# Performance work log

Hardware: AMD Instinct MI355X
Metric: run time of the kernel (lower is better)

The kernel has to match this reference:

```python
import jax, jax.numpy as jnp
import numpy as np

N_CLASS, EMB, HID = 10000, 512, 1024
BATCH, SEQ = 64, 128

_W_NAMES = [
    ("C", (N_CLASS, EMB)),
    ("W_fx", (EMB, HID)), ("W_fh", (HID, HID)),
    ("W_ix", (EMB, HID)), ("W_ih", (HID, HID)),
    ("W_Cx", (EMB, HID)), ("W_Ch", (HID, HID)),
    ("W_ox", (EMB, HID)), ("W_oh", (HID, HID)),
    ("W_fx1", (HID, HID)), ("W_fh1", (HID, HID)),
    ("W_ix1", (HID, HID)), ("W_ih1", (HID, HID)),
    ("W_Cx1", (HID, HID)), ("W_Ch1", (HID, HID)),
    ("W_ox1", (HID, HID)), ("W_oh1", (HID, HID)),
    ("W_out", (HID, N_CLASS)),
]
_B_NAMES = [("b_f", HID), ("b_i", HID), ("b_C", HID), ("b_o", HID),
            ("b_f1", HID), ("b_i1", HID), ("b_C1", HID), ("b_o1", HID),
            ("b_out", N_CLASS)]


def setup_inputs() -> dict:
    key = jax.random.key(0)
    inp = {"X": jax.random.randint(jax.random.fold_in(key, 0), (BATCH, SEQ), 0, N_CLASS)}
    for i, (name, shape) in enumerate(_W_NAMES):
        inp[name] = 0.02 * jax.random.normal(jax.random.fold_in(key, 100 + i), shape, jnp.float32)
    for name, n in _B_NAMES:
        inp[name] = jnp.ones((n,), jnp.float32)  # original inits biases to ones
    return inp


def reference(X, C, W_fx, W_fh, W_ix, W_ih, W_Cx, W_Ch, W_ox, W_oh,
              W_fx1, W_fh1, W_ix1, W_ih1, W_Cx1, W_Ch1, W_ox1, W_oh1,
              W_out, b_f, b_i, b_C, b_o, b_f1, b_i1, b_C1, b_o1, b_out):
    E = jnp.swapaxes(C[X], 0, 1)              # [S, B, emb]
    B = X.shape[0]
    h0 = jnp.zeros((B, W_fh.shape[0]), E.dtype)

    # Layer 0: precompute all input-side gate projections (batched GEMMs).
    xg0 = (E @ W_fx, E @ W_ix, E @ W_Cx, E @ W_ox)  # each [S, B, H]

    def step0(carry, xs):
        h, c = carry
        xf, xi, xc, xo = xs
        f = jax.nn.sigmoid(xf + h @ W_fh + b_f)
        i = jax.nn.sigmoid(xi + h @ W_ih + b_i)
        g = jnp.tanh(xc + h @ W_Ch + b_C)
        c = f * c + i * g
        o = jax.nn.sigmoid(xo + h @ W_oh + b_o)
        h = o * jnp.tanh(c)
        return (h, c), h

    _, H = jax.lax.scan(step0, (h0, h0), xg0)  # H: [S, B, H]

    # Layer 1 (NOTE: original code reuses layer-0 W_ih in the i-gate — kept).
    xg1 = (H @ W_fx1, H @ W_ix1, H @ W_Cx1, H @ W_ox1)

    def step1(carry, xs):
        h, c = carry
        xf, xi, xc, xo = xs
        f = jax.nn.sigmoid(xf + h @ W_fh1 + b_f1)
        i = jax.nn.sigmoid(xi + h @ W_ih + b_i1)
        g = jnp.tanh(xc + h @ W_Ch1 + b_C1)
        c = f * c + i * g
        o = jax.nn.sigmoid(xo + h @ W_oh1 + b_o1)
        h = o * jnp.tanh(c)
        return (h, c), None

    (h1, _), _ = jax.lax.scan(step1, (h0, h0), xg1)
    return h1 @ W_out + b_out                 # [B, n_class]
```

## Files before the change

kernel.cpp:

```cpp
#include <hip/hip_runtime.h>
#include <cstdint>
#include <cstddef>

#define BATCH 64
#define SEQ   128
#define EMB   512
#define HID   1024
#define NCLS  10000
#define NG    4096
#define NOP   10048
#define BH    (BATCH * HID)

typedef __attribute__((ext_vector_type(8))) short short8;
typedef __attribute__((ext_vector_type(4))) short short4v;
typedef __attribute__((ext_vector_type(4))) float floatx4;
typedef unsigned short u16;
typedef unsigned char  u8;

#define RED_PAD    36
#define LDS_BYTES  (8 * 64 * RED_PAD * 4)

__device__ __forceinline__ u16 f2bf(float x) {
    union { float f; unsigned u; } v; v.f = x;
    unsigned r = v.u + 0x7fffu + ((v.u >> 16) & 1u);
    return (u16)(r >> 16);
}
__device__ __forceinline__ float sigm(float x) { return 1.f / (1.f + __expf(-x)); }

__device__ __forceinline__ void wave_wait_range(const unsigned* lines, int lo,
                                                int n, unsigned tgt) {
    const int ln = threadIdx.x & 63;
    const unsigned* p = lines + (size_t)(lo + ln) * 16;
    for (;;) {
        bool ok = true;
        if (ln < n) {
            unsigned v = __hip_atomic_load(p, __ATOMIC_RELAXED, __HIP_MEMORY_SCOPE_AGENT);
            ok = ((v & 255u) >= tgt) && (((v >> 8) & 255u) >= tgt) &&
                 (((v >> 16) & 255u) >= tgt) && ((v >> 24) >= tgt);
        }
        if (__all(ok)) break;
        __builtin_amdgcn_s_sleep(1);
    }
}

__global__ void pack_gates(const float* __restrict__ s0, const float* __restrict__ s1,
                           const float* __restrict__ s2, const float* __restrict__ s3,
                           u16* __restrict__ dst, int kgroups, int kg_off) {
    int t = blockIdx.x * blockDim.x + threadIdx.x;
    if (t >= kgroups * HID) return;
    int u  = t & (HID - 1);
    int kg = t >> 10;
    u16* out = dst + ((size_t)(kg + kg_off) * NG + (size_t)u * 4) * 8;
#pragma unroll
    for (int g = 0; g < 4; ++g) {
        const float* s = (g == 0) ? s0 : (g == 1) ? s1 : (g == 2) ? s2 : s3;
        short8 v;
#pragma unroll
        for (int j = 0; j < 8; ++j)
            v[j] = (short)f2bf(s[(size_t)(kg * 8 + j) * HID + u]);
        *(short8*)(out + g * 8) = v;
    }
}

__global__ void pack_wout(const float* __restrict__ src, u16* __restrict__ dst) {
    int t = blockIdx.x * blockDim.x + threadIdx.x;
    if (t >= 128 * NCLS) return;
    int n  = t % NCLS;
    int kg = t / NCLS;
    short8 v;
#pragma unroll
    for (int j = 0; j < 8; ++j)
        v[j] = (short)f2bf(src[(size_t)(kg * 8 + j) * NCLS + n]);
    *(short8*)(dst + ((size_t)kg * NOP + n) * 8) = v;
}

__global__ void embed_k(const int* __restrict__ X, const float* __restrict__ C,
                        u16* __restrict__ E) {
    const int sb = blockIdx.x;
    const int s = sb >> 6, m = sb & 63;
    const int row = X[m * SEQ + s];
    const floatx4* src = (const floatx4*)(C + (size_t)row * EMB);
    const int t = threadIdx.x;
    floatx4 v = src[t];
    short4v o;
    o[0] = (short)f2bf(v[0]); o[1] = (short)f2bf(v[1]);
    o[2] = (short)f2bf(v[2]); o[3] = (short)f2bf(v[3]);
    u16* dst = E + (size_t)s * (64 * 512) + (size_t)(t >> 1) * 512 + m * 8 + (t & 1) * 4;
    *(short4v*)dst = o;
}

template<int NS, bool WRITE_H>
__device__ __forceinline__ void compute_tick(
    float* __restrict__ redf,
    const short8 (&wreg)[NS][2],
    const short8 (&areg)[NS][4],
    u16* __restrict__ ho, u16* __restrict__ Hout,
    float& c, float bF, float bI, float bC, float bO, int ub)
{
    const int tid = threadIdx.x;
    const int kw = tid >> 6, l = tid & 63;
    const int ml = l & 15, q = l >> 4;

    floatx4 acc[4][2];
#pragma unroll
    for (int mt = 0; mt < 4; ++mt)
#pragma unroll
        for (int ch = 0; ch < 2; ++ch)
            acc[mt][ch] = (floatx4){0.f, 0.f, 0.f, 0.f};

#pragma unroll
    for (int ci = 0; ci < NS; ++ci)
#pragma unroll
        for (int mt = 0; mt < 4; ++mt) {
            acc[mt][0] = __builtin_amdgcn_mfma_f32_16x16x32_bf16(
                areg[ci][mt], wreg[ci][0], acc[mt][0], 0, 0, 0);
            acc[mt][1] = __builtin_amdgcn_mfma_f32_16x16x32_bf16(
                areg[ci][mt], wreg[ci][1], acc[mt][1], 0, 0, 0);
        }

#pragma unroll
    for (int mt = 0; mt < 4; ++mt)
#pragma unroll
        for (int ch = 0; ch < 2; ++ch)
#pragma unroll
            for (int r = 0; r < 4; ++r)
                redf[((size_t)kw * 64 + mt * 16 + q * 4 + r) * RED_PAD + ch * 16 + ml]
                    = acc[mt][ch][r];
    __syncthreads();

    const int m = tid >> 3, u = tid & 7;
    const int nl = u * 4;
    float p0 = 0.f, p1 = 0.f, p2 = 0.f, p3 = 0.f;
#pragma unroll
    for (int k2 = 0; k2 < 8; ++k2) {
        floatx4 rv = *(const floatx4*)&redf[((size_t)k2 * 64 + m) * RED_PAD + nl];
        p0 += rv[0]; p1 += rv[1]; p2 += rv[2]; p3 += rv[3];
    }
    float f = sigm(p0 + bF);
    float i = sigm(p1 + bI);
    float g = tanhf(p2 + bC);
    float o = sigm(p3 + bO);
    float cc = f * c + i * g;
    c = cc;
    u16 hb = f2bf(o * tanhf(cc));
    __hip_atomic_store(&ho[(size_t)ub * 512 + tid], hb,
                       __ATOMIC_RELAXED, __HIP_MEMORY_SCOPE_AGENT);
    if (WRITE_H)
        __hip_atomic_store(&Hout[(size_t)ub * 512 + tid], hb,
                           __ATOMIC_RELAXED, __HIP_MEMORY_SCOPE_AGENT);
}

struct PArgs {
    const u16 *E, *Wcat0, *Wcat1;
    u16 *H, *h0c, *h1c;
    const float *b_f, *b_i, *b_C, *b_o, *b_f1, *b_i1, *b_C1, *b_o1;
    unsigned* sync;
};

__global__ void __launch_bounds__(512, 2) persist_k(PArgs a) {
    extern __shared__ float redf[];

    const int b   = blockIdx.x;
    const int ub  = b & 127;
    const int tid = threadIdx.x;
    const bool L0 = (b < 128);

    const int kw = tid >> 6, l = tid & 63;
    const int ml = l & 15, q = l >> 4;

    const int ug = ub * 8 + (tid & 7);
    const float bF = L0 ? a.b_f[ug] : a.b_f1[ug];
    const float bI = L0 ? a.b_i[ug] : a.b_i1[ug];
    const float bC = L0 ? a.b_C[ug] : a.b_C1[ug];
    const float bO = L0 ? a.b_o[ug] : a.b_o1[ug];
    float c = 0.f;

    unsigned* flags0_u32 = a.sync;
    unsigned* flags1_u32 = a.sync + 1024;
    u8* my0 = (u8*)a.sync + (size_t)(ub >> 2) * 64 + (ub & 3);
    u8* my1 = (u8*)a.sync + 4096 + (size_t)(ub >> 2) * 64 + (ub & 3);

    if (L0) {
        short8 wreg[6][2];
#pragma unroll
        for (int ci = 0; ci < 6; ++ci)
#pragma unroll
            for (int ch = 0; ch < 2; ++ch) {
                const int kg = (kw * 6 + ci) * 4 + q;
                wreg[ci][ch] = *(const short8*)(
                    a.Wcat0 + ((size_t)kg * NG + ub * 32 + ch * 16 + ml) * 8);
            }
        const int Sl   = kw * 6 + 5;
        const bool hasH = (Sl >= 16);
        const int flo  = (kw * 6 > 16) ? (kw * 6 - 16) : 0;
        const int fcnt = hasH ? (Sl - 16 - flo + 1) : 0;

        for (int t = 0; t < 128; ++t) {
            short8 areg[6][4];
            const u16* Et  = a.E   + (size_t)t * (64 * 512);
            const u16* hin = a.h0c + (size_t)t * BH;
#pragma unroll
            for (int ci = 0; ci < 6; ++ci) {
                const int S = kw * 6 + ci;
                if (S < 16) {
                    const int kg = S * 4 + q;
#pragma unroll
                    for (int mt = 0; mt < 4; ++mt)
                        areg[ci][mt] = *(const short8*)(
                            Et + (size_t)kg * 512 + (mt * 16 + ml) * 8);
                }
            }
            if (hasH && t > 0) wave_wait_range(flags0_u32, flo, fcnt, (unsigned)t);
            asm volatile("" ::: "memory");
#pragma unroll
            for (int ci = 0; ci < 6; ++ci) {
                const int S = kw * 6 + ci;
                if (S >= 16) {
                    const int kg = (S - 16) * 4 + q;
#pragma unroll
                    for (int mt = 0; mt < 4; ++mt)
                        areg[ci][mt] = *(const short8*)(
                            hin + (size_t)kg * 512 + (mt * 16 + ml) * 8);
                }
            }
            __builtin_amdgcn_sched_barrier(0);
            compute_tick<6, true>(redf, wreg, areg,
                                  a.h0c + (size_t)(t + 1) * BH,
                                  a.H + (size_t)t * BH,
                                  c, bF, bI, bC, bO, ub);
            asm volatile("s_waitcnt vmcnt(0)" ::: "memory");
            __syncthreads();
            if (tid == 0)
                __hip_atomic_store(my0, (u8)(t + 1),
                                   __ATOMIC_RELAXED, __HIP_MEMORY_SCOPE_AGENT);
        }
    } else {
        short8 wreg[8][2];
#pragma unroll
        for (int ci = 0; ci < 8; ++ci)
#pragma unroll
            for (int ch = 0; ch < 2; ++ch) {
                const int kg = (kw * 8 + ci) * 4 + q;
                wreg[ci][ch] = *(const short8*)(
                    a.Wcat1 + ((size_t)kg * NG + ub * 32 + ch * 16 + ml) * 8);
            }
        const int kg0 = (kw & 3) * 8;

        for (int s = 0; s < 128; ++s) {
            short8 areg[8][4];
            const u16* src;
            if (kw >= 4) {
                if (s > 0) wave_wait_range(flags1_u32, kg0, 8, (unsigned)s);
                src = a.h1c + (size_t)s * BH;
            } else {
                wave_wait_range(flags0_u32, kg0, 8, (unsigned)(s + 1));
                src = a.H + (size_t)s * BH;
            }
            asm volatile("" ::: "memory");
#pragma unroll
            for (int ci = 0; ci < 8; ++ci) {
                const int kg = (kg0 + ci) * 4 + q;
#pragma unroll
                for (int mt = 0; mt < 4; ++mt)
                    areg[ci][mt] = *(const short8*)(
                        src + (size_t)kg * 512 + (mt * 16 + ml) * 8);
            }
            __builtin_amdgcn_sched_barrier(0);
            compute_tick<8, false>(redf, wreg, areg,
                                   a.h1c + (size_t)(s + 1) * BH, nullptr,
                                   c, bF, bI, bC, bO, ub);
            asm volatile("s_waitcnt vmcnt(0)" ::: "memory");
            __syncthreads();
            if (tid == 0)
                __hip_atomic_store(my1, (u8)(s + 1),
                                   __ATOMIC_RELAXED, __HIP_MEMORY_SCOPE_AGENT);
        }
    }
}

__global__ void __launch_bounds__(256) out_gemm(
    const u16* __restrict__ h1, const u16* __restrict__ W,
    const float* __restrict__ bout, float* __restrict__ out)
{
    __shared__ float red[4][64][33];
    const int tid = threadIdx.x;
    const int w = tid >> 6, l = tid & 63;
    const int ml = l & 15, q = l >> 4;
    const int n0 = blockIdx.x * 32;

    floatx4 acc[4][2];
#pragma unroll
    for (int mi = 0; mi < 4; ++mi)
#pragma unroll
        for (int ni = 0; ni < 2; ++ni)
            acc[mi][ni] = (floatx4){0.f, 0.f, 0.f, 0.f};

#pragma unroll
    for (int ci = 0; ci < 8; ++ci) {
        const int k = (ci * 4 + w) << 5;
        const int kg = (k >> 3) + q;
        const u16* ar = h1 + (size_t)kg * 512 + ml * 8;
        short8 a0 = *(const short8*)(ar);
        short8 a1 = *(const short8*)(ar + 16 * 8);
        short8 a2 = *(const short8*)(ar + 32 * 8);
        short8 a3 = *(const short8*)(ar + 48 * 8);
        const u16* br = W + ((size_t)((k >> 3) + q) * NOP + n0 + ml) * 8;
        short8 b0 = *(const short8*)(br);
        short8 b1 = *(const short8*)(br + 16 * 8);
        acc[0][0] = __builtin_amdgcn_mfma_f32_16x16x32_bf16(a0, b0, acc[0][0], 0, 0, 0);
        acc[1][0] = __builtin_amdgcn_mfma_f32_16x16x32_bf16(a1, b0, acc[1][0], 0, 0, 0);
        acc[2][0] = __builtin_amdgcn_mfma_f32_16x16x32_bf16(a2, b0, acc[2][0], 0, 0, 0);
        acc[3][0] = __builtin_amdgcn_mfma_f32_16x16x32_bf16(a3, b0, acc[3][0], 0, 0, 0);
        acc[0][1] = __builtin_amdgcn_mfma_f32_16x16x32_bf16(a0, b1, acc[0][1], 0, 0, 0);
        acc[1][1] = __builtin_amdgcn_mfma_f32_16x16x32_bf16(a1, b1, acc[1][1], 0, 0, 0);
        acc[2][1] = __builtin_amdgcn_mfma_f32_16x16x32_bf16(a2, b1, acc[2][1], 0, 0, 0);
        acc[3][1] = __builtin_amdgcn_mfma_f32_16x16x32_bf16(a3, b1, acc[3][1], 0, 0, 0);
    }

#pragma unroll
    for (int mi = 0; mi < 4; ++mi)
#pragma unroll
        for (int ni = 0; ni < 2; ++ni)
#pragma unroll
            for (int r = 0; r < 4; ++r)
                red[w][mi * 16 + q * 4 + r][ni * 16 + ml] = acc[mi][ni][r];
    __syncthreads();

    const int m = tid >> 2;
#pragma unroll
    for (int jj = 0; jj < 8; ++jj) {
        const int nl = (tid & 3) * 8 + jj;
        const int n = n0 + nl;
        if (n < NCLS) {
            float v = red[0][m][nl] + red[1][m][nl] + red[2][m][nl] + red[3][m][nl] + bout[n];
            out[(size_t)m * NCLS + n] = v;
        }
    }
}

extern "C" void kernel_launch(void* const* d_in, const int* in_sizes, int n_in,
                              void* d_out, int out_size, void* d_ws, size_t ws_size,
                              hipStream_t stream) {
    (void)in_sizes; (void)n_in; (void)out_size; (void)ws_size;
    const int*   X     = (const int*)  d_in[0];
    const float* C     = (const float*)d_in[1];
    const float* W_fx  = (const float*)d_in[2];
    const float* W_fh  = (const float*)d_in[3];
    const float* W_ix  = (const float*)d_in[4];
    const float* W_ih  = (const float*)d_in[5];
    const float* W_Cx  = (const float*)d_in[6];
    const float* W_Ch  = (const float*)d_in[7];
    const float* W_ox  = (const float*)d_in[8];
    const float* W_oh  = (const float*)d_in[9];
    const float* W_fx1 = (const float*)d_in[10];
    const float* W_fh1 = (const float*)d_in[11];
    const float* W_ix1 = (const float*)d_in[12];
    const float* W_Cx1 = (const float*)d_in[14];
    const float* W_Ch1 = (const float*)d_in[15];
    const float* W_ox1 = (const float*)d_in[16];
    const float* W_oh1 = (const float*)d_in[17];
    const float* W_out = (const float*)d_in[18];
    const float* b_f   = (const float*)d_in[19];
    const float* b_i   = (const float*)d_in[20];
    const float* b_C   = (const float*)d_in[21];
    const float* b_o   = (const float*)d_in[22];
    const float* b_f1  = (const float*)d_in[23];
    const float* b_i1  = (const float*)d_in[24];
    const float* b_C1  = (const float*)d_in[25];
    const float* b_o1  = (const float*)d_in[26];
    const float* b_out = (const float*)d_in[27];
    float* out = (float*)d_out;

    uint8_t* ws = (uint8_t*)d_ws;
    const size_t SZ_WCAT0 = (size_t)1536 * NG * 2;
    const size_t SZ_WCAT1 = (size_t)2048 * NG * 2;
    const size_t SZ_WOUTP = (size_t)1024 * NOP * 2;
    const size_t SZ_E     = (size_t)SEQ * BATCH * EMB * 2;
    const size_t SZ_H     = (size_t)SEQ * BH * 2;
    const size_t SZ_HC    = (size_t)(SEQ + 1) * BH * 2;
    u16*   Wcat0 = (u16*)ws;                         ws += SZ_WCAT0;
    u16*   Wcat1 = (u16*)ws;                         ws += SZ_WCAT1;
    u16*   WoutP = (u16*)ws;                         ws += SZ_WOUTP;
    u16*   E     = (u16*)ws;                         ws += SZ_E;
    u16*   H     = (u16*)ws;                         ws += SZ_H;
    u16*   h0c   = (u16*)ws;                         ws += SZ_HC;
    u16*   h1c   = (u16*)ws;                         ws += SZ_HC;
    unsigned* syncw = (unsigned*)ws;                 ws += 8192;

    hipFuncSetAttribute((const void*)persist_k,
                        hipFuncAttributeMaxDynamicSharedMemorySize, LDS_BYTES);

    pack_gates<<<256, 256, 0, stream>>>(W_fx, W_ix, W_Cx, W_ox, Wcat0, 64, 0);
    pack_gates<<<512, 256, 0, stream>>>(W_fh, W_ih, W_Ch, W_oh, Wcat0, 128, 64);
    pack_gates<<<512, 256, 0, stream>>>(W_fx1, W_ix1, W_Cx1, W_ox1, Wcat1, 128, 0);
    pack_gates<<<512, 256, 0, stream>>>(W_fh1, W_ih, W_Ch1, W_oh1, Wcat1, 128, 128);
    hipMemsetAsync(WoutP, 0, SZ_WOUTP, stream);
    pack_wout<<<(128 * NCLS + 255) / 256, 256, 0, stream>>>(W_out, WoutP);
    embed_k<<<SEQ * BATCH, 128, 0, stream>>>(X, C, E);

    hipMemsetAsync(h0c, 0, (size_t)BH * 2, stream);
    hipMemsetAsync(h1c, 0, (size_t)BH * 2, stream);
    hipMemsetAsync(syncw, 0, 8192, stream);

    PArgs pa;
    pa.E = E; pa.Wcat0 = Wcat0; pa.Wcat1 = Wcat1;
    pa.H = H; pa.h0c = h0c; pa.h1c = h1c;
    pa.b_f = b_f; pa.b_i = b_i; pa.b_C = b_C; pa.b_o = b_o;
    pa.b_f1 = b_f1; pa.b_i1 = b_i1; pa.b_C1 = b_C1; pa.b_o1 = b_o1;
    pa.sync = syncw;
    persist_k<<<256, 512, LDS_BYTES, stream>>>(pa);

    out_gemm<<<314, 256, 0, stream>>>(h1c + (size_t)SEQ * BH, WoutP, b_out, out);
}
```

Measured before the change: 959.4 us.

## Replace per-block barrier flag with per-wave stamps and double-buffered reduction LDS

Each wave now stores its own progress byte after its h writes complete. This removes the trailing __syncthreads and the single-thread flag store each timestep. The reduction scratch in LDS is double-buffered by step parity so the next tick's writes cannot race the previous tick's reads without a second barrier. Waiters poll 64-bit words covering 8 wave stamps per block, so each lane checks more flags. The risks are doubled LDS use, which could affect the two-blocks-per-CU occupancy, and the correctness of the finer-grained producer/consumer synchronization.

```diff
diff --git a/kernel.cpp b/kernel.cpp
--- a/kernel.cpp
+++ b/kernel.cpp
@@ -16,9 +16,11 @@
 typedef __attribute__((ext_vector_type(4))) float floatx4;
 typedef unsigned short u16;
 typedef unsigned char  u8;
+typedef unsigned long long u64;
 
 #define RED_PAD    36
-#define LDS_BYTES  (8 * 64 * RED_PAD * 4)
+#define RED_SIZE   (8 * 64 * RED_PAD)
+#define LDS_BYTES  (2 * RED_SIZE * 4)
 
 __device__ __forceinline__ u16 f2bf(float x) {
     union { float f; unsigned u; } v; v.f = x;
@@ -26,18 +28,25 @@
     return (u16)(r >> 16);
 }
 __device__ __forceinline__ float sigm(float x) { return 1.f / (1.f + __expf(-x)); }
-
-__device__ __forceinline__ void wave_wait_range(const unsigned* lines, int lo,
-                                                int n, unsigned tgt) {
+__device__ __forceinline__ unsigned umin2(unsigned a, unsigned b) { return a < b ? a : b; }
+
+__device__ __forceinline__ bool ok8(u64 v, unsigned tgt) {
+    unsigned a = (unsigned)v, b = (unsigned)(v >> 32);
+    unsigned m = umin2(umin2(a & 255u, (a >> 8) & 255u),
+                       umin2((a >> 16) & 255u, a >> 24));
+    unsigned n = umin2(umin2(b & 255u, (b >> 8) & 255u),
+                       umin2((b >> 16) & 255u, b >> 24));
+    return umin2(m, n) >= tgt;
+}
+
+__device__ __forceinline__ void wave_wait_blocks(const u64* flags, int lo,
+                                                 int n, unsigned tgt) {
     const int ln = threadIdx.x & 63;
-    const unsigned* p = lines + (size_t)(lo + ln) * 16;
+    const u64* p = flags + lo + ln;
     for (;;) {
         bool ok = true;
-        if (ln < n) {
-            unsigned v = __hip_atomic_load(p, __ATOMIC_RELAXED, __HIP_MEMORY_SCOPE_AGENT);
-            ok = ((v & 255u) >= tgt) && (((v >> 8) & 255u) >= tgt) &&
-                 (((v >> 16) & 255u) >= tgt) && ((v >> 24) >= tgt);
-        }
+        if (ln < n)
+            ok = ok8(__hip_atomic_load(p, __ATOMIC_RELAXED, __HIP_MEMORY_SCOPE_AGENT), tgt);
         if (__all(ok)) break;
         __builtin_amdgcn_s_sleep(1);
     }
@@ -91,10 +100,11 @@
 
 template<int NS, bool WRITE_H>
 __device__ __forceinline__ void compute_tick(
-    float* __restrict__ redf,
+    float* __restrict__ redb,
     const short8 (&wreg)[NS][2],
     const short8 (&areg)[NS][4],
     u16* __restrict__ ho, u16* __restrict__ Hout,
+    u8* __restrict__ stamp, unsigned sval,
     float& c, float bF, float bI, float bC, float bO, int ub)
 {
     const int tid = threadIdx.x;
@@ -124,16 +134,19 @@
         for (int ch = 0; ch < 2; ++ch)
 #pragma unroll
             for (int r = 0; r < 4; ++r)
-                redf[((size_t)kw * 64 + mt * 16 + q * 4 + r) * RED_PAD + ch * 16 + ml]
+                redb[((size_t)kw * 64 + mt * 16 + q * 4 + r) * RED_PAD + ch * 16 + ml]
                     = acc[mt][ch][r];
-    __syncthreads();
+
+    asm volatile("s_waitcnt lgkmcnt(0)" ::: "memory");
+    __builtin_amdgcn_s_barrier();
+    __builtin_amdgcn_sched_barrier(0);
 
     const int m = tid >> 3, u = tid & 7;
     const int nl = u * 4;
     float p0 = 0.f, p1 = 0.f, p2 = 0.f, p3 = 0.f;
 #pragma unroll
     for (int k2 = 0; k2 < 8; ++k2) {
-        floatx4 rv = *(const floatx4*)&redf[((size_t)k2 * 64 + m) * RED_PAD + nl];
+        floatx4 rv = *(const floatx4*)&redb[((size_t)k2 * 64 + m) * RED_PAD + nl];
         p0 += rv[0]; p1 += rv[1]; p2 += rv[2]; p3 += rv[3];
     }
     float f = sigm(p0 + bF);
@@ -148,6 +161,11 @@
     if (WRITE_H)
         __hip_atomic_store(&Hout[(size_t)ub * 512 + tid], hb,
                            __ATOMIC_RELAXED, __HIP_MEMORY_SCOPE_AGENT);
+
+    asm volatile("s_waitcnt vmcnt(0)" ::: "memory");
+    if (l == 0)
+        __hip_atomic_store(stamp + kw, (u8)sval,
+                           __ATOMIC_RELAXED, __HIP_MEMORY_SCOPE_AGENT);
 }
 
 struct PArgs {
@@ -157,7 +175,9 @@
     unsigned* sync;
 };
 
-__global__ void __launch_bounds__(512, 2) persist_k(PArgs a) {
+__global__ void __launch_bounds__(512, 2)
+__attribute__((amdgpu_waves_per_eu(2, 2)))
+persist_k(PArgs a) {
     extern __shared__ float redf[];
 
     const int b   = blockIdx.x;
@@ -175,10 +195,10 @@
     const float bO = L0 ? a.b_o[ug] : a.b_o1[ug];
     float c = 0.f;
 
-    unsigned* flags0_u32 = a.sync;
-    unsigned* flags1_u32 = a.sync + 1024;
-    u8* my0 = (u8*)a.sync + (size_t)(ub >> 2) * 64 + (ub & 3);
-    u8* my1 = (u8*)a.sync + 4096 + (size_t)(ub >> 2) * 64 + (ub & 3);
+    const u64* flags0 = (const u64*)a.sync;
+    const u64* flags1 = (const u64*)((u8*)a.sync + 4096);
+    u8* my0 = (u8*)a.sync + (size_t)ub * 8;
+    u8* my1 = (u8*)a.sync + 4096 + (size_t)ub * 8;
 
     if (L0) {
         short8 wreg[6][2];
@@ -190,10 +210,11 @@
                 wreg[ci][ch] = *(const short8*)(
                     a.Wcat0 + ((size_t)kg * NG + ub * 32 + ch * 16 + ml) * 8);
             }
-        const int Sl   = kw * 6 + 5;
-        const bool hasH = (Sl >= 16);
-        const int flo  = (kw * 6 > 16) ? (kw * 6 - 16) : 0;
-        const int fcnt = hasH ? (Sl - 16 - flo + 1) : 0;
+        const int Smax = kw * 6 + 5;
+        const int Smin = (kw * 6 > 16) ? kw * 6 : 16;
+        const bool hasH = (Smax >= 16);
+        const int blo  = hasH ? (Smin - 16) * 4 : 0;
+        const int bn   = hasH ? (Smax - Smin + 1) * 4 : 0;
 
         for (int t = 0; t < 128; ++t) {
             short8 areg[6][4];
@@ -210,7 +231,8 @@
                             Et + (size_t)kg * 512 + (mt * 16 + ml) * 8);
                 }
             }
-            if (hasH && t > 0) wave_wait_range(flags0_u32, flo, fcnt, (unsigned)t);
+            asm volatile("" ::: "memory");
+            if (hasH && t > 0) wave_wait_blocks(flags0, blo, bn, (unsigned)t);
             asm volatile("" ::: "memory");
 #pragma unroll
             for (int ci = 0; ci < 6; ++ci) {
@@ -224,15 +246,11 @@
                 }
             }
             __builtin_amdgcn_sched_barrier(0);
-            compute_tick<6, true>(redf, wreg, areg,
+            compute_tick<6, true>(redf + (size_t)(t & 1) * RED_SIZE, wreg, areg,
                                   a.h0c + (size_t)(t + 1) * BH,
                                   a.H + (size_t)t * BH,
+                                  my0, (unsigned)(t + 1),
                                   c, bF, bI, bC, bO, ub);
-            asm volatile("s_waitcnt vmcnt(0)" ::: "memory");
-            __syncthreads();
-            if (tid == 0)
-                __hip_atomic_store(my0, (u8)(t + 1),
-                                   __ATOMIC_RELAXED, __HIP_MEMORY_SCOPE_AGENT);
         }
     } else {
         short8 wreg[8][2];
@@ -245,15 +263,16 @@
                     a.Wcat1 + ((size_t)kg * NG + ub * 32 + ch * 16 + ml) * 8);
             }
         const int kg0 = (kw & 3) * 8;
+        const int blo = kg0 * 4;
 
         for (int s = 0; s < 128; ++s) {
             short8 areg[8][4];
             const u16* src;
             if (kw >= 4) {
-                if (s > 0) wave_wait_range(flags1_u32, kg0, 8, (unsigned)s);
+                if (s > 0) wave_wait_blocks(flags1, blo, 32, (unsigned)s);
                 src = a.h1c + (size_t)s * BH;
             } else {
-                wave_wait_range(flags0_u32, kg0, 8, (unsigned)(s + 1));
+                wave_wait_blocks(flags0, blo, 32, (unsigned)(s + 1));
                 src = a.H + (size_t)s * BH;
             }
             asm volatile("" ::: "memory");
@@ -266,14 +285,10 @@
                         src + (size_t)kg * 512 + (mt * 16 + ml) * 8);
             }
             __builtin_amdgcn_sched_barrier(0);
-            compute_tick<8, false>(redf, wreg, areg,
+            compute_tick<8, false>(redf + (size_t)(s & 1) * RED_SIZE, wreg, areg,
                                    a.h1c + (size_t)(s + 1) * BH, nullptr,
+                                   my1, (unsigned)(s + 1),
                                    c, bF, bI, bC, bO, ub);
-            asm volatile("s_waitcnt vmcnt(0)" ::: "memory");
-            __syncthreads();
-            if (tid == 0)
-                __hip_atomic_store(my1, (u8)(s + 1),
-                                   __ATOMIC_RELAXED, __HIP_MEMORY_SCOPE_AGENT);
         }
     }
 }
```

Result: slower. 2.464 ms (+156.9%).
